# Kernel optimization log

Measured on AMD Instinct MI355X. Metric: run time of the kernel, lower is better.

## Reference

```python
import jax, jax.numpy as jnp
import numpy as np

D_MODEL = 512
OUT_MODEL = 512
NUM_HEADS = 8
D_K = OUT_MODEL // NUM_HEADS


def setup_inputs() -> dict:
    key = jax.random.key(0)
    ks = jax.random.split(key, 11)
    B, S = 4, 2048
    inp = {
        "Q": jax.random.normal(ks[0], (B, S, D_MODEL), dtype=jnp.float32),
        "K": jax.random.normal(ks[1], (B, S, D_MODEL), dtype=jnp.float32),
        "V": jax.random.normal(ks[2], (B, S, D_MODEL), dtype=jnp.float32),
    }
    sc = 1.0 / np.sqrt(D_MODEL)
    inp["Wq"] = jax.random.normal(ks[3], (D_MODEL, OUT_MODEL), dtype=jnp.float32) * sc
    inp["bq"] = jnp.zeros((OUT_MODEL,), dtype=jnp.float32)
    inp["Wk"] = jax.random.normal(ks[4], (D_MODEL, OUT_MODEL), dtype=jnp.float32) * sc
    inp["bk"] = jnp.zeros((OUT_MODEL,), dtype=jnp.float32)
    inp["Wv"] = jax.random.normal(ks[5], (D_MODEL, OUT_MODEL), dtype=jnp.float32) * sc
    inp["bv"] = jnp.zeros((OUT_MODEL,), dtype=jnp.float32)
    inp["Wo"] = jax.random.normal(ks[6], (OUT_MODEL, OUT_MODEL), dtype=jnp.float32) * sc
    inp["bo"] = jnp.zeros((OUT_MODEL,), dtype=jnp.float32)
    return inp


def _split_heads(x):
    B, S, _ = x.shape
    return x.reshape(B, S, NUM_HEADS, D_K).transpose(0, 2, 1, 3)  # [B,H,S,Dk]


def reference(Q, K, V, Wq, bq, Wk, bk, Wv, bv, Wo, bo):
    q = _split_heads(Q @ Wq + bq)
    k = _split_heads(K @ Wk + bk)
    v = _split_heads(V @ Wv + bv)
    scores = jnp.einsum("bhsd,bhtd->bhst", q, k) / jnp.sqrt(jnp.float32(D_K))
    probs = jax.nn.softmax(scores, axis=-1)
    attn = jnp.einsum("bhst,bhtd->bhsd", probs, v)  # [B,H,S,Dk]
    B, H, S, Dk = attn.shape
    merged = attn.transpose(0, 2, 1, 3).reshape(B, S, OUT_MODEL)
    return merged @ Wo + bo
```

## Files before the change

### kernel.cpp

```cpp
#include <hip/hip_runtime.h>
#include <hip/hip_bf16.h>
#include <cstdint>


using short8 = __attribute__((ext_vector_type(8))) short;
using f32x4  = __attribute__((ext_vector_type(4))) float;
using f32x16 = __attribute__((ext_vector_type(16))) float;

#define DEVINL __device__ __forceinline__

constexpr int BB  = 4;
constexpr int SS  = 2048;
constexpr int DM  = 512;
constexpr int NH  = 8;
constexpr int DKH = 64;
constexpr float C2 = 0.18033688011112042f;

DEVINL unsigned short f2bf(float f) {
    __hip_bfloat16 h = __float2bfloat16(f);
    return *reinterpret_cast<unsigned short*>(&h);
}

DEVINL f32x4 mfma16(short8 a, short8 b, f32x4 c) {
    return __builtin_amdgcn_mfma_f32_16x16x32_bf16(a, b, c, 0, 0, 0);
}
DEVINL f32x16 mfma32(short8 a, short8 b, f32x16 c) {
    return __builtin_amdgcn_mfma_f32_32x32x16_bf16(a, b, c, 0, 0, 0);
}

DEVINL void gl16(const void* g, void* l) {
    __builtin_amdgcn_global_load_lds(
        (const __attribute__((address_space(1))) unsigned int*)g,
        (__attribute__((address_space(3))) unsigned int*)l, 16, 0, 0);
}
DEVINL void vmcnt0() { asm volatile("s_waitcnt vmcnt(0)" ::: "memory"); }
#define WAIT_VM(N) asm volatile("s_waitcnt vmcnt(" #N ")" ::: "memory")
DEVINL void barrier() { __builtin_amdgcn_s_barrier(); }

DEVINL unsigned cvtpk(float a, float b) {
    unsigned r;
    asm("v_cvt_pk_bf16_f32 %0, %1, %2" : "=v"(r) : "v"(a), "v"(b));
    return r;
}

__global__ __launch_bounds__(256)
void prep_w(const float* __restrict__ Wq, const float* __restrict__ Wk,
            const float* __restrict__ Wv, const float* __restrict__ Wo,
            unsigned short* __restrict__ wt)
{
    const int z = blockIdx.z;
    const float* W = (z == 0) ? Wq : (z == 1) ? Wk : (z == 2) ? Wv : Wo;
    unsigned short* Wtz = wt + (size_t)z * DM * DM;

    __shared__ unsigned short T[64][72];
    const int t = threadIdx.x;
    const int k0 = blockIdx.x * 64, n0 = blockIdx.y * 64;
    const int r = t >> 2, cs = t & 3;

    #pragma unroll
    for (int q = 0; q < 4; ++q) {
        float4 v = *reinterpret_cast<const float4*>(
            &W[(size_t)(k0 + r) * DM + n0 + cs * 16 + q * 4]);
        union { unsigned short u[4]; unsigned long long ll; } pk;
        pk.u[0] = f2bf(v.x); pk.u[1] = f2bf(v.y);
        pk.u[2] = f2bf(v.z); pk.u[3] = f2bf(v.w);
        *reinterpret_cast<unsigned long long*>(&T[r][cs * 16 + q * 4]) = pk.ll;
    }
    __syncthreads();
    union { unsigned short u[8]; short8 v; } p0, p1;
    #pragma unroll
    for (int e = 0; e < 8; ++e) p0.u[e] = T[cs * 16 + e][r];
    #pragma unroll
    for (int e = 0; e < 8; ++e) p1.u[e] = T[cs * 16 + 8 + e][r];
    *reinterpret_cast<short8*>(&Wtz[(size_t)(n0 + r) * DM + k0 + cs * 16]) = p0.v;
    *reinterpret_cast<short8*>(&Wtz[(size_t)(n0 + r) * DM + k0 + cs * 16 + 8]) = p1.v;
}

__global__ __launch_bounds__(256, 4)
void qkv_proj_kernel(const float* __restrict__ Qin, const float* __restrict__ Kin,
                     const float* __restrict__ Vin,
                     const unsigned short* __restrict__ wt,
                     const float* __restrict__ bq, const float* __restrict__ bk,
                     const float* __restrict__ bv,
                     unsigned short* __restrict__ qb, unsigned short* __restrict__ kb2,
                     unsigned short* __restrict__ vt2)
{
    const int z = blockIdx.z;
    const float* A           = (z == 0) ? Qin : (z == 1) ? Kin : Vin;
    const unsigned short* Wt = wt + (size_t)z * DM * DM;
    const float* bias        = (z == 0) ? bq : (z == 1) ? bk : bv;

    __shared__ unsigned short SMEM[16384];

    const int tid = threadIdx.x, lane = tid & 63, w = tid >> 6;
    const int wm = w >> 1, wn = w & 1;
    const int row16 = lane & 15, kg = lane >> 4;
    const int m0tok = blockIdx.x * 128, n0ch = blockIdx.y * 128;

    const int ar = tid >> 1, ah = tid & 1;

    float4 apf[4];
    auto load_A = [&](int kt) {
        const float* Ap = &A[(size_t)(m0tok + ar) * DM + kt * 32 + ah * 16];
        #pragma unroll
        for (int q = 0; q < 4; ++q)
            apf[q] = *reinterpret_cast<const float4*>(Ap + q * 4);
    };
    auto write_A = [&](int buf) {
        #pragma unroll
        for (int s = 0; s < 2; ++s) {
            union { unsigned short u[8]; short8 v; } pk;
            float4 a = apf[2 * s], b = apf[2 * s + 1];
            pk.u[0] = f2bf(a.x); pk.u[1] = f2bf(a.y);
            pk.u[2] = f2bf(a.z); pk.u[3] = f2bf(a.w);
            pk.u[4] = f2bf(b.x); pk.u[5] = f2bf(b.y);
            pk.u[6] = f2bf(b.z); pk.u[7] = f2bf(b.w);
            int phys = (ah * 2 + s) ^ (ar & 3);
            *reinterpret_cast<short8*>(&SMEM[buf * 4096 + ar * 32 + phys * 8]) = pk.v;
        }
    };
    auto issue_B = [&](int kt, int buf) {
        #pragma unroll
        for (int i = 0; i < 2; ++i) {
            int chunk = tid + i * 256;
            int n = chunk >> 2, c = chunk & 3;
            const unsigned short* src =
                &Wt[(size_t)(n0ch + n) * DM + kt * 32 + ((c ^ (n & 3)) * 8)];
            gl16(src, (char*)SMEM + 16384 + (size_t)buf * 8192 +
                      (size_t)(w * 64 + i * 256) * 16);
        }
    };

    f32x4 acc[4][4] = {};
    const int aoff = ((z == 2) ? wn : wm) * 64;
    const int boff = ((z == 2) ? wm : wn) * 64;

    load_A(0); issue_B(0, 0);
    vmcnt0();
    write_A(0);
    __syncthreads();

    for (int t = 0; t < 16; ++t) {
        const int cur = t & 1, nxt = cur ^ 1;
        if (t + 1 < 16) { issue_B(t + 1, nxt); load_A(t + 1); }

        short8 af[4], bfr[4];
        #pragma unroll
        for (int i = 0; i < 4; ++i) {
            int ra = aoff + i * 16 + row16;
            int rb = boff + i * 16 + row16;
            af[i]  = *reinterpret_cast<const short8*>(
                &SMEM[cur * 4096 + ra * 32 + ((kg ^ (ra & 3)) * 8)]);
            bfr[i] = *reinterpret_cast<const short8*>(
                &SMEM[8192 + cur * 4096 + rb * 32 + ((kg ^ (rb & 3)) * 8)]);
        }
        __builtin_amdgcn_s_setprio(1);
        #pragma unroll
        for (int mf = 0; mf < 4; ++mf)
            #pragma unroll
            for (int nf = 0; nf < 4; ++nf)
                acc[mf][nf] = (z == 2)
                    ? mfma16(bfr[mf], af[nf], acc[mf][nf])
                    : mfma16(af[mf], bfr[nf], acc[mf][nf]);
        __builtin_amdgcn_s_setprio(0);

        vmcnt0();
        if (t + 1 < 16) write_A(nxt);
        __syncthreads();
    }

    if (z == 0) {
        #pragma unroll
        for (int nf = 0; nf < 4; ++nf) {
            int ch = n0ch + wn * 64 + nf * 16 + row16;
            float bval = bias[ch];
            int h = ch >> 6, dk = ch & 63;
            #pragma unroll
            for (int mf = 0; mf < 4; ++mf)
                #pragma unroll
                for (int j = 0; j < 4; ++j) {
                    int tok = m0tok + wm * 64 + mf * 16 + kg * 4 + j;
                    int b = tok >> 11, s = tok & 2047;
                    qb[(((size_t)b * NH + h) * SS + s) * DKH + dk] =
                        f2bf((acc[mf][nf][j] + bval) * C2);
                }
        }
    } else {
        __syncthreads();
        if (z == 1) {
            #pragma unroll
            for (int nf = 0; nf < 4; ++nf) {
                int dk = nf * 16 + row16;
                float bval = bias[n0ch + wn * 64 + dk];
                #pragma unroll
                for (int mf = 0; mf < 4; ++mf)
                    #pragma unroll
                    for (int j = 0; j < 4; ++j) {
                        int s6 = mf * 16 + kg * 4 + j;
                        SMEM[w * 4096 + (dk >> 3) * 512 + s6 * 8 + (dk & 7)] =
                            f2bf(acc[mf][nf][j] + bval);
                    }
            }
        } else {
            const int tile = wn * 2 + wm;
            #pragma unroll
            for (int mf = 0; mf < 4; ++mf)
                #pragma unroll
                for (int j = 0; j < 4; ++j) {
                    int dk6 = mf * 16 + kg * 4 + j;
                    float bval = bias[n0ch + wm * 64 + dk6];
                    #pragma unroll
                    for (int nf = 0; nf < 4; ++nf) {
                        int s6 = nf * 16 + row16;
                        SMEM[tile * 4096 + (s6 >> 3) * 512 + dk6 * 8 + (s6 & 7)] =
                            f2bf(acc[mf][nf][j] + bval);
                    }
                }
        }
        __syncthreads();
        const int sblk = m0tok + (w >> 1) * 64;
        const int hg   = (n0ch >> 6) + (w & 1);
        const int b    = sblk >> 11, s_in_b = sblk & 2047;
        unsigned short* dst =
            ((z == 1) ? kb2 : vt2) +
            ((size_t)(b * NH + hg)) * (SS * DKH) + (size_t)(s_in_b >> 6) * 4096;
        #pragma unroll
        for (int i = 0; i < 8; ++i)
            *reinterpret_cast<short8*>(&dst[i * 512 + lane * 8]) =
                *reinterpret_cast<const short8*>(&SMEM[w * 4096 + i * 512 + lane * 8]);
    }
}

__global__ __launch_bounds__(256, 2)
void attn_kernel(const unsigned short* __restrict__ qb,
                 const unsigned short* __restrict__ kb2,
                 const unsigned short* __restrict__ vt2,
                 unsigned short* __restrict__ am)
{
    __shared__ unsigned short Ks[3][4096];
    __shared__ unsigned short Vs[3][4096];

    const int tid = threadIdx.x, lane = tid & 63, w = tid >> 6;
    const int l31 = lane & 31, hi = lane >> 5;
    const int bh = blockIdx.y, b = bh >> 3, h = bh & 7;
    const int q0 = blockIdx.x * 128;
    const size_t base = (size_t)bh * (SS * DKH);

    auto stage_KV = [&](int tt, int buf) {
        const unsigned short* ksrc = kb2 + base + (size_t)tt * 4096;
        const unsigned short* vsrc = vt2 + base + (size_t)tt * 4096;
        #pragma unroll
        for (int i = 0; i < 2; ++i) {
            int cb = i * 256 + w * 64;
            gl16(ksrc + (size_t)(cb + lane) * 8, (char*)Ks[buf] + (size_t)cb * 16);
            gl16(vsrc + (size_t)(cb + lane) * 8, (char*)Vs[buf] + (size_t)cb * 16);
        }
    };

    short8 qf[4];
    const int qrow = q0 + w * 32 + l31;
    #pragma unroll
    for (int ks = 0; ks < 4; ++ks)
        qf[ks] = *reinterpret_cast<const short8*>(
            &qb[base + (size_t)qrow * DKH + (ks * 2 + hi) * 8]);
    vmcnt0();

    stage_KV(0, 0);
    stage_KV(1, 1);
    WAIT_VM(4);
    barrier();

    f32x16 o[2] = {};
    float lsum = 0.f;

    for (int tt = 0; tt < 32; ++tt) {
        const int cur = tt % 3;
        if (tt + 2 < 32) stage_KV(tt + 2, (tt + 2) % 3);

        f32x16 sfr[2] = {};
        __builtin_amdgcn_s_setprio(1);
        #pragma unroll
        for (int ks = 0; ks < 4; ++ks) {
            int c = ks * 2 + hi;
            #pragma unroll
            for (int mkv = 0; mkv < 2; ++mkv) {
                short8 kf = *reinterpret_cast<const short8*>(
                    &Ks[cur][(c * 64 + mkv * 32 + l31) * 8]);
                sfr[mkv] = mfma32(kf, qf[ks], sfr[mkv]);
            }
        }
        __builtin_amdgcn_s_setprio(0);

        unsigned pk[2][4][2];
        #pragma unroll
        for (int mkv = 0; mkv < 2; ++mkv)
            #pragma unroll
            for (int bq = 0; bq < 4; ++bq) {
                float p0 = __builtin_amdgcn_exp2f(sfr[mkv][bq * 4 + 0]);
                float p1 = __builtin_amdgcn_exp2f(sfr[mkv][bq * 4 + 1]);
                float p2 = __builtin_amdgcn_exp2f(sfr[mkv][bq * 4 + 2]);
                float p3 = __builtin_amdgcn_exp2f(sfr[mkv][bq * 4 + 3]);
                lsum += (p0 + p1) + (p2 + p3);
                pk[mkv][bq][0] = cvtpk(p0, p1);
                pk[mkv][bq][1] = cvtpk(p2, p3);
            }

        __builtin_amdgcn_s_setprio(1);
        #pragma unroll
        for (int ks2 = 0; ks2 < 4; ++ks2) {
            const int mkv = ks2 >> 1, b0 = (ks2 & 1) * 2, b1 = b0 + 1;
            unsigned x0 = pk[mkv][b0][0], y0 = pk[mkv][b1][0];
            unsigned x1 = pk[mkv][b0][1], y1 = pk[mkv][b1][1];
            asm volatile("v_permlane32_swap_b32 %0, %1" : "+v"(x0), "+v"(y0));
            asm volatile("v_permlane32_swap_b32 %0, %1" : "+v"(x1), "+v"(y1));
            union { unsigned u[4]; short8 s; } pa;
            pa.u[0] = x0; pa.u[1] = x1; pa.u[2] = y0; pa.u[3] = y1;
            int c = ks2 * 2 + hi;
            #pragma unroll
            for (int ndk = 0; ndk < 2; ++ndk) {
                short8 vf = *reinterpret_cast<const short8*>(
                    &Vs[cur][(c * 64 + ndk * 32 + l31) * 8]);
                o[ndk] = mfma32(pa.s, vf, o[ndk]);
            }
        }
        __builtin_amdgcn_s_setprio(0);

        if (tt + 2 < 32)      { WAIT_VM(4); }
        else if (tt + 1 < 32) { WAIT_VM(0); }
        if (tt + 1 < 32) barrier();
    }

    float lfull = lsum + __shfl_xor(lsum, 32, 64);
    float linv = 1.0f / lfull;
    #pragma unroll
    for (int r = 0; r < 16; ++r) {
        int qloc = (r & 3) + 8 * (r >> 2) + 4 * hi;
        float li = __shfl(linv, qloc, 64);
        int sg = q0 + w * 32 + qloc;
        #pragma unroll
        for (int ndk = 0; ndk < 2; ++ndk) {
            int dk = ndk * 32 + l31;
            am[((size_t)b * SS + sg) * DM + h * DKH + dk] =
                f2bf(o[ndk][r] * li);
        }
    }
}

__global__ __launch_bounds__(256, 4)
void out_proj_kernel(const unsigned short* __restrict__ am,
                     const unsigned short* __restrict__ Wt,
                     const float* __restrict__ bo,
                     float* __restrict__ out)
{
    __shared__ unsigned short As[2][64 * 32];
    __shared__ unsigned short Bs[2][128 * 32];

    const int tid = threadIdx.x, lane = tid & 63, w = tid >> 6;
    const int wm = w & 1, wn = w >> 1;
    const int row16 = lane & 15, kg = lane >> 4;
    const int m0 = blockIdx.x * 64;
    const int n0 = blockIdx.y * 128;

    auto stage = [&](int kt, int buf) {
        {
            int r = tid >> 2, c = tid & 3;
            gl16(&am[(size_t)(m0 + r) * DM + kt * 32 + ((c ^ (r & 3)) * 8)],
                 (char*)As + (size_t)buf * 4096 + (size_t)(w * 64) * 16);
        }
        #pragma unroll
        for (int i = 0; i < 2; ++i) {
            int cc = tid + i * 256;
            int n = cc >> 2, c = cc & 3;
            gl16(&Wt[(size_t)(n0 + n) * DM + kt * 32 + ((c ^ (n & 3)) * 8)],
                 (char*)Bs + (size_t)buf * 8192 + (size_t)(w * 64 + i * 256) * 16);
        }
    };

    f32x4 acc[2][4] = {};

    stage(0, 0);
    vmcnt0();
    __syncthreads();

    for (int t = 0; t < 16; ++t) {
        const int cur = t & 1, nxt = cur ^ 1;
        if (t + 1 < 16) stage(t + 1, nxt);

        short8 af[2], bfr[4];
        #pragma unroll
        for (int i = 0; i < 2; ++i) {
            int ra = wm * 32 + i * 16 + row16;
            af[i] = *reinterpret_cast<const short8*>(
                &As[cur][ra * 32 + ((kg ^ (ra & 3)) * 8)]);
        }
        #pragma unroll
        for (int i = 0; i < 4; ++i) {
            int rb = wn * 64 + i * 16 + row16;
            bfr[i] = *reinterpret_cast<const short8*>(
                &Bs[cur][rb * 32 + ((kg ^ (rb & 3)) * 8)]);
        }
        __builtin_amdgcn_s_setprio(1);
        #pragma unroll
        for (int mf = 0; mf < 2; ++mf)
            #pragma unroll
            for (int nf = 0; nf < 4; ++nf)
                acc[mf][nf] = mfma16(af[mf], bfr[nf], acc[mf][nf]);
        __builtin_amdgcn_s_setprio(0);

        vmcnt0();
        __syncthreads();
    }

    #pragma unroll
    for (int nf = 0; nf < 4; ++nf) {
        int n = n0 + wn * 64 + nf * 16 + row16;
        float bval = bo[n];
        #pragma unroll
        for (int mf = 0; mf < 2; ++mf)
            #pragma unroll
            for (int j = 0; j < 4; ++j) {
                int mrow = m0 + wm * 32 + mf * 16 + kg * 4 + j;
                out[(size_t)mrow * DM + n] = acc[mf][nf][j] + bval;
            }
    }
}

extern "C" void kernel_launch(void* const* d_in, const int* in_sizes, int n_in,
                              void* d_out, int out_size, void* d_ws, size_t ws_size,
                              hipStream_t stream) {
    const float* Q  = (const float*)d_in[0];
    const float* K  = (const float*)d_in[1];
    const float* V  = (const float*)d_in[2];
    const float* Wq = (const float*)d_in[3];
    const float* bq = (const float*)d_in[4];
    const float* Wk = (const float*)d_in[5];
    const float* bk = (const float*)d_in[6];
    const float* Wv = (const float*)d_in[7];
    const float* bv = (const float*)d_in[8];
    const float* Wo = (const float*)d_in[9];
    const float* bo = (const float*)d_in[10];
    float* out = (float*)d_out;

    const size_t per = (size_t)BB * NH * SS * DKH;
    unsigned short* qb  = (unsigned short*)d_ws;
    unsigned short* kb2 = qb + per;
    unsigned short* vt2 = kb2 + per;
    unsigned short* am  = vt2 + per;
    unsigned short* wt  = am + per;

    prep_w<<<dim3(8, 8, 4), 256, 0, stream>>>(Wq, Wk, Wv, Wo, wt);
    qkv_proj_kernel<<<dim3(64, 4, 3), 256, 0, stream>>>(
        Q, K, V, wt, bq, bk, bv, qb, kb2, vt2);
    attn_kernel<<<dim3(SS / 128, BB * NH), 256, 0, stream>>>(qb, kb2, vt2, am);
    out_proj_kernel<<<dim3(128, 4), 256, 0, stream>>>(
        am, wt + 3 * (size_t)DM * DM, bo, out);
}
```

Baseline: 89.37 us.

## Software-pipeline attention loop: overlap QK of next tile with PV of previous

Restructures the flash-attention inner loop so the QK^T matrix multiply for tile tt runs back-to-back with the PV multiply for tile tt-1, and the exp/softmax conversion runs afterward. The goal is to let MFMA work overlap the transcendental and pack work instead of serializing within each tile. V gets a fourth LDS buffer to hold the delayed tile, which raises shared memory per block and keeps the packed probabilities live across iterations, adding register pressure.

```diff
diff --git a/kernel.cpp b/kernel.cpp
--- a/kernel.cpp
+++ b/kernel.cpp
@@ -238,7 +238,7 @@
                  unsigned short* __restrict__ am)
 {
     __shared__ unsigned short Ks[3][4096];
-    __shared__ unsigned short Vs[3][4096];
+    __shared__ unsigned short Vs[4][4096];
 
     const int tid = threadIdx.x, lane = tid & 63, w = tid >> 6;
     const int l31 = lane & 31, hi = lane >> 5;
@@ -246,14 +246,15 @@
     const int q0 = blockIdx.x * 128;
     const size_t base = (size_t)bh * (SS * DKH);
 
-    auto stage_KV = [&](int tt, int buf) {
+    auto stage_KV = [&](int tt) {
         const unsigned short* ksrc = kb2 + base + (size_t)tt * 4096;
         const unsigned short* vsrc = vt2 + base + (size_t)tt * 4096;
+        const int kbuf = tt % 3, vbuf = tt & 3;
         #pragma unroll
         for (int i = 0; i < 2; ++i) {
             int cb = i * 256 + w * 64;
-            gl16(ksrc + (size_t)(cb + lane) * 8, (char*)Ks[buf] + (size_t)cb * 16);
-            gl16(vsrc + (size_t)(cb + lane) * 8, (char*)Vs[buf] + (size_t)cb * 16);
+            gl16(ksrc + (size_t)(cb + lane) * 8, (char*)Ks[kbuf] + (size_t)cb * 16);
+            gl16(vsrc + (size_t)(cb + lane) * 8, (char*)Vs[vbuf] + (size_t)cb * 16);
         }
     };
 
@@ -265,33 +266,28 @@
             &qb[base + (size_t)qrow * DKH + (ks * 2 + hi) * 8]);
     vmcnt0();
 
-    stage_KV(0, 0);
-    stage_KV(1, 1);
+    stage_KV(0);
+    stage_KV(1);
     WAIT_VM(4);
     barrier();
 
     f32x16 o[2] = {};
     float lsum = 0.f;
-
-    for (int tt = 0; tt < 32; ++tt) {
-        const int cur = tt % 3;
-        if (tt + 2 < 32) stage_KV(tt + 2, (tt + 2) % 3);
-
-        f32x16 sfr[2] = {};
-        __builtin_amdgcn_s_setprio(1);
+    unsigned pk[2][4][2];
+
+    auto do_QK = [&](int kcur, f32x16 (&sfr)[2]) {
         #pragma unroll
         for (int ks = 0; ks < 4; ++ks) {
             int c = ks * 2 + hi;
             #pragma unroll
             for (int mkv = 0; mkv < 2; ++mkv) {
                 short8 kf = *reinterpret_cast<const short8*>(
-                    &Ks[cur][(c * 64 + mkv * 32 + l31) * 8]);
+                    &Ks[kcur][(c * 64 + mkv * 32 + l31) * 8]);
                 sfr[mkv] = mfma32(kf, qf[ks], sfr[mkv]);
             }
         }
-        __builtin_amdgcn_s_setprio(0);
-
-        unsigned pk[2][4][2];
+    };
+    auto do_softmax = [&](const f32x16 (&sfr)[2]) {
         #pragma unroll
         for (int mkv = 0; mkv < 2; ++mkv)
             #pragma unroll
@@ -304,8 +300,8 @@
                 pk[mkv][bq][0] = cvtpk(p0, p1);
                 pk[mkv][bq][1] = cvtpk(p2, p3);
             }
-
-        __builtin_amdgcn_s_setprio(1);
+    };
+    auto do_PV = [&](int vbuf) {
         #pragma unroll
         for (int ks2 = 0; ks2 < 4; ++ks2) {
             const int mkv = ks2 >> 1, b0 = (ks2 & 1) * 2, b1 = b0 + 1;
@@ -319,16 +315,38 @@
             #pragma unroll
             for (int ndk = 0; ndk < 2; ++ndk) {
                 short8 vf = *reinterpret_cast<const short8*>(
-                    &Vs[cur][(c * 64 + ndk * 32 + l31) * 8]);
+                    &Vs[vbuf][(c * 64 + ndk * 32 + l31) * 8]);
                 o[ndk] = mfma32(pa.s, vf, o[ndk]);
             }
         }
+    };
+
+    {
+        stage_KV(2);
+        f32x16 sfr[2] = {};
+        __builtin_amdgcn_s_setprio(1);
+        do_QK(0, sfr);
         __builtin_amdgcn_s_setprio(0);
+        do_softmax(sfr);
+        WAIT_VM(4);
+        barrier();
+    }
+
+    for (int tt = 1; tt < 32; ++tt) {
+        if (tt + 2 < 32) stage_KV(tt + 2);
+
+        f32x16 sfr[2] = {};
+        __builtin_amdgcn_s_setprio(1);
+        do_QK(tt % 3, sfr);
+        do_PV((tt - 1) & 3);
+        __builtin_amdgcn_s_setprio(0);
+        do_softmax(sfr);
 
         if (tt + 2 < 32)      { WAIT_VM(4); }
         else if (tt + 1 < 32) { WAIT_VM(0); }
         if (tt + 1 < 32) barrier();
     }
+    do_PV(31 & 3);
 
     float lfull = lsum + __shfl_xor(lsum, 32, 64);
     float linv = 1.0f / lfull;
```

Measured after the change: 86.88 us. 2.8% less time.
